# Optimization experiments

Hardware: AMD Instinct MI355X
Metric: run time of the kernel (lower is better)

## Reference

```python
import jax, jax.numpy as jnp
import numpy as np


def setup_inputs() -> dict:
    key = jax.random.key(0)
    k1, k2, k3 = jax.random.split(key, 3)
    b, n, d, f = 16, 2048, 256, 256
    features = jax.random.normal(k1, (b, n, d), dtype=jnp.float32)
    # dense adjacency; row-normalize like MeanAggregator's normalized A
    A = jax.random.uniform(k2, (b, n, n), dtype=jnp.float32)
    A = A / jnp.sum(A, axis=-1, keepdims=True)
    weight = jax.random.normal(k3, (2 * d, f), dtype=jnp.float32) * (1.0 / np.sqrt(2 * d))
    bias = jnp.zeros((f,), dtype=jnp.float32)
    return {"features": features, "A": A, "weight": weight, "bias": bias}


def reference(features, A, weight, bias):
    # agg = A @ features  (MeanAggregator: row-normalized adjacency)
    agg = jnp.einsum('bnm,bmd->bnd', A, features)  # [b,n,d]
    d = features.shape[-1]
    # split-weight GEMM instead of materializing concat:
    # [feat, agg] @ W == feat @ W[:d] + agg @ W[d:]
    out = (jnp.einsum('bnd,df->bnf', features, weight[:d])
           + jnp.einsum('bnd,df->bnf', agg, weight[d:])
           + bias)
    return jax.nn.relu(out)
```

## Files before the change

kernel.cpp:

```cpp
#include <hip/hip_runtime.h>

typedef __attribute__((ext_vector_type(8))) short bf16x8;
typedef __attribute__((ext_vector_type(4))) float f32x4;

__device__ __forceinline__ unsigned short f2bf(float f) {
    unsigned int u = __builtin_bit_cast(unsigned int, f);
    unsigned int r = (u + 0x7FFFu + ((u >> 16) & 1u)) >> 16;
    return (unsigned short)r;
}
__device__ __forceinline__ unsigned int pkbf(float lo, float hi) {
    unsigned int ul = __builtin_bit_cast(unsigned int, lo) + 0x8000u;
    unsigned int uh = __builtin_bit_cast(unsigned int, hi) + 0x8000u;
    return (uh & 0xFFFF0000u) | (ul >> 16);
}
__device__ __forceinline__ float bf2f(unsigned short u) {
    unsigned int x = ((unsigned int)u) << 16;
    return __builtin_bit_cast(float, x);
}

__device__ __forceinline__ void gll16(const void* g, void* l) {
    __builtin_amdgcn_global_load_lds(
        (const __attribute__((address_space(1))) void*)g,
        (__attribute__((address_space(3))) void*)l, 16, 0, 0);
}

__global__ __launch_bounds__(256) void transpose_cvt_kernel(
    const float* __restrict__ src, unsigned short* __restrict__ dstT,
    unsigned short* __restrict__ dstS, int R, int C)
{
    __shared__ float tile[64][65];
    const int b = blockIdx.z;
    const float* s = src + (size_t)b * R * C;
    const int r0 = blockIdx.x * 64, c0 = blockIdx.y * 64;
    const int t = threadIdx.x;
    const int r = t >> 2, cg = (t & 3) * 16;

    float v[16];
    const float4* p = reinterpret_cast<const float4*>(s + (size_t)(r0 + r) * C + c0 + cg);
#pragma unroll
    for (int i = 0; i < 4; ++i) {
        float4 q = p[i];
        v[4 * i + 0] = q.x; v[4 * i + 1] = q.y; v[4 * i + 2] = q.z; v[4 * i + 3] = q.w;
    }
#pragma unroll
    for (int i = 0; i < 16; ++i) tile[r][cg + i] = v[i];

    if (dstS) {
        unsigned int w[8];
#pragma unroll
        for (int i = 0; i < 8; ++i)
            w[i] = (unsigned)f2bf(v[2 * i]) | ((unsigned)f2bf(v[2 * i + 1]) << 16);
        unsigned int* d = reinterpret_cast<unsigned int*>(
            dstS + (size_t)b * R * C + (size_t)(r0 + r) * C + c0 + cg);
        *reinterpret_cast<uint4*>(d)     = make_uint4(w[0], w[1], w[2], w[3]);
        *reinterpret_cast<uint4*>(d + 4) = make_uint4(w[4], w[5], w[6], w[7]);
    }

    __syncthreads();

    const int cl = t >> 2, rg = (t & 3) * 16;
    unsigned int w[8];
#pragma unroll
    for (int i = 0; i < 8; ++i) {
        unsigned short lo = f2bf(tile[rg + 2 * i][cl]);
        unsigned short hi = f2bf(tile[rg + 2 * i + 1][cl]);
        w[i] = (unsigned)lo | ((unsigned)hi << 16);
    }
    unsigned int* d = reinterpret_cast<unsigned int*>(
        dstT + (size_t)b * R * C + (size_t)(c0 + cl) * R + r0 + rg);
    *reinterpret_cast<uint4*>(d)     = make_uint4(w[0], w[1], w[2], w[3]);
    *reinterpret_cast<uint4*>(d + 4) = make_uint4(w[4], w[5], w[6], w[7]);
}

__global__ __launch_bounds__(256, 2) void kpre_gemm(
    const float* __restrict__ F, const unsigned short* __restrict__ Wt,
    const float* __restrict__ bias, unsigned short* __restrict__ H,
    unsigned short* __restrict__ Gt)
{
    __shared__ __align__(16) short Fb[64 * 256];
    __shared__ __align__(16) short Wb[256 * 64];

    const int tid = threadIdx.x;
    const int lane = tid & 63, wid = tid >> 6;
    const int lo = lane & 15, hi = lane >> 4;
    const int rb = blockIdx.x;
    const int batch = rb >> 5;
    const int mb = (rb & 31) * 64;
    const size_t m0g = (size_t)rb * 64;

    {
        const int frow = tid >> 2, fq = tid & 3;
        const float* fp = F + (m0g + frow) * 256 + fq * 64;
#pragma unroll
        for (int g = 0; g < 2; ++g) {
            float4 q[8];
#pragma unroll
            for (int i = 0; i < 8; ++i)
                q[i] = reinterpret_cast<const float4*>(fp)[g * 8 + i];
#pragma unroll
            for (int j = 0; j < 4; ++j) {
                unsigned int w0 = pkbf(q[2*j].x,   q[2*j].y);
                unsigned int w1 = pkbf(q[2*j].z,   q[2*j].w);
                unsigned int w2 = pkbf(q[2*j+1].x, q[2*j+1].y);
                unsigned int w3 = pkbf(q[2*j+1].z, q[2*j+1].w);
                int slot = fq * 8 + g * 4 + j;
                int off = frow * 256 + ((slot ^ (frow & 7)) << 3);
                *reinterpret_cast<uint4*>(&Fb[off]) = make_uint4(w0, w1, w2, w3);
            }
        }
    }

    f32x4 acc[4][4];

#pragma unroll
    for (int pass = 0; pass < 2; ++pass) {
#pragma unroll
        for (int m = 0; m < 4; ++m)
#pragma unroll
            for (int n = 0; n < 4; ++n) acc[m][n] = (f32x4){0.f, 0.f, 0.f, 0.f};

        for (int kt = 0; kt < 4; ++kt) {
            const int kbase = pass * 256 + kt * 64;
#pragma unroll
            for (int it = 0; it < 8; ++it) {
                int si = it * 256 + tid;
                int row = si >> 3, slot = si & 7;
                const unsigned short* g = Wt + (size_t)row * 512 + kbase + ((slot ^ (row & 7)) << 3);
                gll16(g, Wb + (size_t)si * 8);
            }
            __syncthreads();

#pragma unroll
            for (int kk = 0; kk < 2; ++kk) {
                bf16x8 af[4], bw[4];
#pragma unroll
                for (int m = 0; m < 4; ++m) {
                    int row = m * 16 + lo;
                    int slot = kt * 8 + kk * 4 + hi;
                    af[m] = *reinterpret_cast<const bf16x8*>(&Fb[row * 256 + ((slot ^ (row & 7)) << 3)]);
                }
#pragma unroll
                for (int n = 0; n < 4; ++n) {
                    int row = wid * 64 + n * 16 + lo;
                    bw[n] = *reinterpret_cast<const bf16x8*>(&Wb[row * 64 + (((kk * 4 + hi) ^ (row & 7)) << 3)]);
                }
#pragma unroll
                for (int m = 0; m < 4; ++m)
#pragma unroll
                    for (int n = 0; n < 4; ++n)
                        acc[m][n] = __builtin_amdgcn_mfma_f32_16x16x32_bf16(af[m], bw[n], acc[m][n], 0, 0, 0);
            }
            __syncthreads();
        }

        if (pass == 0) {
            float bv[4];
#pragma unroll
            for (int n = 0; n < 4; ++n) bv[n] = bias[wid * 64 + n * 16 + lo];
            unsigned short* Hb = H + m0g * 256;
#pragma unroll
            for (int m = 0; m < 4; ++m)
#pragma unroll
                for (int n = 0; n < 4; ++n)
#pragma unroll
                    for (int j = 0; j < 4; ++j) {
                        int row = m * 16 + hi * 4 + j;
                        int col = wid * 64 + n * 16 + lo;
                        Hb[(size_t)row * 256 + col] = f2bf(acc[m][n][j] + bv[n]);
                    }
        } else {
            short* T = Wb + wid * 4096;
#pragma unroll
            for (int m = 0; m < 4; ++m)
#pragma unroll
                for (int n = 0; n < 4; ++n)
#pragma unroll
                    for (int j = 0; j < 4; ++j) {
                        int gr = m * 16 + hi * 4 + j;
                        int gc = n * 16 + lo;
                        int slot = gr >> 3, e = gr & 7;
                        T[gc * 64 + ((slot ^ (gc & 7)) << 3) + e] = f2bf(acc[m][n][j]);
                    }
            unsigned short* Gb = Gt + ((size_t)batch * 256 + wid * 64) * 2048 + mb;
#pragma unroll
            for (int i = 0; i < 8; ++i) {
                int f = i * 8 + (lane >> 3);
                int s = lane & 7;
                bf16x8 v = *reinterpret_cast<const bf16x8*>(&T[f * 64 + ((s ^ (f & 7)) << 3)]);
                *reinterpret_cast<bf16x8*>(Gb + (size_t)f * 2048 + s * 8) = v;
            }
        }
    }
}

__global__ __launch_bounds__(512, 2) void kmain_gemm(
    const float* __restrict__ A, const unsigned short* __restrict__ Gt,
    const unsigned short* __restrict__ H, float* __restrict__ out)
{
    __shared__ __align__(16) short Ab[2][128 * 64];
    __shared__ __align__(16) short Bb[2][256 * 64];

    const int tid = threadIdx.x;
    const int lane = tid & 63, wid = tid >> 6;
    const int wr = wid >> 2, wc = wid & 3;
    const int lo = lane & 15, hi = lane >> 4;

    const int bid = blockIdx.x;
    const int wg = ((bid & 7) << 5) | (bid >> 3);
    const int batch = wg >> 4;
    const int mt    = wg & 15;

    const float* Abase = A + ((size_t)batch * 2048 + (size_t)mt * 128) * 2048;
    const unsigned short* Gbase = Gt + (size_t)batch * 256 * 2048;

    const int arow = tid >> 2;
    const int acg  = tid & 3;

    f32x4 acc[4][4];
#pragma unroll
    for (int m = 0; m < 4; ++m)
#pragma unroll
        for (int n = 0; n < 4; ++n) acc[m][n] = (f32x4){0.f, 0.f, 0.f, 0.f};

    float4 qa0[4], qa1[4];

    auto loadA = [&](float4* q, int k0) {
        const float4* p4 = reinterpret_cast<const float4*>(
            Abase + (size_t)arow * 2048 + k0);
#pragma unroll
        for (int i = 0; i < 4; ++i) q[i] = p4[acg + 4 * i];
    };
    auto writeA = [&](int buf, const float4* q) {
#pragma unroll
        for (int i = 0; i < 4; ++i) {
            uint2 w;
            w.x = pkbf(q[i].x, q[i].y);
            w.y = pkbf(q[i].z, q[i].w);
            int s = 2 * i + (acg >> 1);
            int off = arow * 64 + ((s ^ (arow & 7)) << 3) + (acg & 1) * 4;
            *reinterpret_cast<uint2*>(&Ab[buf][off]) = w;
        }
    };
    auto stageB = [&](int buf, int k0) {
#pragma unroll
        for (int it = 0; it < 4; ++it) {
            int si = it * 512 + tid;
            int row = si >> 3, slot = si & 7;
            const unsigned short* g = Gbase + (size_t)row * 2048 + k0 + ((slot ^ (row & 7)) << 3);
            gll16(g, &Bb[buf][(size_t)si * 8]);
        }
    };
    auto compute = [&](int buf) {
#pragma unroll
        for (int kk = 0; kk < 2; ++kk) {
            bf16x8 af[4], bfv[4];
#pragma unroll
            for (int m = 0; m < 4; ++m) {
                int row = wr * 64 + m * 16 + lo;
                af[m] = *reinterpret_cast<const bf16x8*>(
                    &Ab[buf][row * 64 + (((kk * 4 + hi) ^ (row & 7)) << 3)]);
            }
#pragma unroll
            for (int n = 0; n < 4; ++n) {
                int row = wc * 64 + n * 16 + lo;
                bfv[n] = *reinterpret_cast<const bf16x8*>(
                    &Bb[buf][row * 64 + (((kk * 4 + hi) ^ (row & 7)) << 3)]);
            }
            __builtin_amdgcn_s_setprio(1);
#pragma unroll
            for (int m = 0; m < 4; ++m)
#pragma unroll
                for (int n = 0; n < 4; ++n)
                    acc[m][n] = __builtin_amdgcn_mfma_f32_16x16x32_bf16(af[m], bfv[n], acc[m][n], 0, 0, 0);
            __builtin_amdgcn_s_setprio(0);
        }
    };

    loadA(qa0, 0);
    stageB(0, 0);
    writeA(0, qa0);
    loadA(qa1, 64);
    asm volatile("s_waitcnt vmcnt(4) lgkmcnt(0)" ::: "memory");
    __builtin_amdgcn_s_barrier();
    asm volatile("" ::: "memory");
    stageB(1, 64);

    for (int tt = 0; tt < 15; ++tt) {
        const int t0 = tt * 2;
        writeA(1, qa1);
        loadA(qa0, (t0 + 2) * 64);
        compute(0);
        asm volatile("s_waitcnt vmcnt(4) lgkmcnt(0)" ::: "memory");
        __builtin_amdgcn_s_barrier();
        asm volatile("" ::: "memory");
        stageB(0, (t0 + 2) * 64);
        writeA(0, qa0);
        loadA(qa1, (t0 + 3) * 64);
        compute(1);
        asm volatile("s_waitcnt vmcnt(4) lgkmcnt(0)" ::: "memory");
        __builtin_amdgcn_s_barrier();
        asm volatile("" ::: "memory");
        stageB(1, (t0 + 3) * 64);
    }
    writeA(1, qa1);
    compute(0);
    asm volatile("s_waitcnt vmcnt(0) lgkmcnt(0)" ::: "memory");
    __builtin_amdgcn_s_barrier();
    asm volatile("" ::: "memory");
    compute(1);

    const size_t rowbase = (size_t)batch * 2048 + (size_t)mt * 128;
    const unsigned short* Hb = H + rowbase * 256;
    float* obase = out + rowbase * 256;
#pragma unroll
    for (int m = 0; m < 4; ++m) {
#pragma unroll
        for (int n = 0; n < 4; ++n) {
            int col = wc * 64 + n * 16 + lo;
#pragma unroll
            for (int j = 0; j < 4; ++j) {
                int row = wr * 64 + m * 16 + hi * 4 + j;
                float v = acc[m][n][j] + bf2f(Hb[(size_t)row * 256 + col]);
                obase[(size_t)row * 256 + col] = fmaxf(v, 0.f);
            }
        }
    }
}

extern "C" void kernel_launch(void* const* d_in, const int* in_sizes, int n_in,
                              void* d_out, int out_size, void* d_ws, size_t ws_size,
                              hipStream_t stream) {
    const float* features = (const float*)d_in[0];
    const float* A        = (const float*)d_in[1];
    const float* weight   = (const float*)d_in[2];
    const float* bias     = (const float*)d_in[3];
    float* out = (float*)d_out;

    const size_t WT_B = (size_t)256 * 512 * 2;
    const size_t H_B  = (size_t)32768 * 256 * 2;
    const size_t GT_B = (size_t)16 * 256 * 2048 * 2;
    if (ws_size < WT_B + H_B + GT_B) return;

    char* ws = (char*)d_ws;
    unsigned short* Wt = (unsigned short*)ws;
    unsigned short* H  = (unsigned short*)(ws + WT_B);
    unsigned short* Gt = (unsigned short*)(ws + WT_B + H_B);

    dim3 gW(512 / 64, 256 / 64, 1);
    transpose_cvt_kernel<<<gW, 256, 0, stream>>>(weight, Wt, nullptr, 512, 256);

    kpre_gemm<<<512, 256, 0, stream>>>(features, Wt, bias, H, Gt);

    kmain_gemm<<<256, 512, 0, stream>>>(A, Gt, H, out);
}
```

Before: 111.4 us.

## Split main GEMM output columns across two blocks with deeper K tiles

The main aggregation GEMM now tiles the output as 128x128 instead of 128x256, doubling the grid to 512 blocks, and raises the K step from 64 to 128 with a 16-slot XOR swizzle. The A-tile load is also reorganized so each wave reads whole rows with coalesced float4 accesses. The goal is more blocks in flight and fewer barriers per K. The cost is that each fp32 A row tile is now read and converted twice, once per column half, which doubles traffic on the largest input.

New measurement: 113.6 us. About the same (+2.0%).

```diff
diff --git a/kernel.cpp b/kernel.cpp
--- a/kernel.cpp
+++ b/kernel.cpp
@@ -197,8 +197,8 @@
     const float* __restrict__ A, const unsigned short* __restrict__ Gt,
     const unsigned short* __restrict__ H, float* __restrict__ out)
 {
-    __shared__ __align__(16) short Ab[2][128 * 64];
-    __shared__ __align__(16) short Bb[2][256 * 64];
+    __shared__ __align__(16) short Ab[2][128 * 128];
+    __shared__ __align__(16) short Bb[2][128 * 128];
 
     const int tid = threadIdx.x;
     const int lane = tid & 63, wid = tid >> 6;
@@ -206,38 +206,40 @@
     const int lo = lane & 15, hi = lane >> 4;
 
     const int bid = blockIdx.x;
-    const int wg = ((bid & 7) << 5) | (bid >> 3);
-    const int batch = wg >> 4;
-    const int mt    = wg & 15;
+    const int wg = ((bid & 7) << 6) | (bid >> 3);
+    const int batch = wg >> 5;
+    const int mt    = (wg >> 1) & 15;
+    const int nt    = wg & 1;
 
     const float* Abase = A + ((size_t)batch * 2048 + (size_t)mt * 128) * 2048;
-    const unsigned short* Gbase = Gt + (size_t)batch * 256 * 2048;
-
-    const int arow = tid >> 2;
-    const int acg  = tid & 3;
-
-    f32x4 acc[4][4];
+    const unsigned short* Gbase = Gt + ((size_t)batch * 256 + (size_t)nt * 128) * 2048;
+
+    f32x4 acc[4][2];
 #pragma unroll
     for (int m = 0; m < 4; ++m)
 #pragma unroll
-        for (int n = 0; n < 4; ++n) acc[m][n] = (f32x4){0.f, 0.f, 0.f, 0.f};
-
-    float4 qa0[4], qa1[4];
-
-    auto loadA = [&](float4* q, int k0) {
-        const float4* p4 = reinterpret_cast<const float4*>(
-            Abase + (size_t)arow * 2048 + k0);
-#pragma unroll
-        for (int i = 0; i < 4; ++i) q[i] = p4[acg + 4 * i];
+        for (int n = 0; n < 2; ++n) acc[m][n] = (f32x4){0.f, 0.f, 0.f, 0.f};
+
+    float4 qa[8];
+
+    auto loadA = [&](int k0) {
+        const float* base = Abase + k0;
+#pragma unroll
+        for (int i = 0; i < 8; ++i) {
+            int r = (wid << 4) + (i << 1) + (lane >> 5);
+            qa[i] = reinterpret_cast<const float4*>(base + (size_t)r * 2048)[lane & 31];
+        }
     };
-    auto writeA = [&](int buf, const float4* q) {
-#pragma unroll
-        for (int i = 0; i < 4; ++i) {
+    auto writeA = [&](int buf) {
+#pragma unroll
+        for (int i = 0; i < 8; ++i) {
+            int r = (wid << 4) + (i << 1) + (lane >> 5);
+            int c32 = lane & 31;
+            int slot = c32 >> 1, half = c32 & 1;
+            int off = r * 128 + (((slot ^ (r & 15)) << 3) + half * 4);
             uint2 w;
-            w.x = pkbf(q[i].x, q[i].y);
-            w.y = pkbf(q[i].z, q[i].w);
-            int s = 2 * i + (acg >> 1);
-            int off = arow * 64 + ((s ^ (arow & 7)) << 3) + (acg & 1) * 4;
+            w.x = pkbf(qa[i].x, qa[i].y);
+            w.y = pkbf(qa[i].z, qa[i].w);
             *reinterpret_cast<uint2*>(&Ab[buf][off]) = w;
         }
     };
@@ -245,64 +247,57 @@
 #pragma unroll
         for (int it = 0; it < 4; ++it) {
             int si = it * 512 + tid;
-            int row = si >> 3, slot = si & 7;
-            const unsigned short* g = Gbase + (size_t)row * 2048 + k0 + ((slot ^ (row & 7)) << 3);
+            int row = si >> 4, slot = si & 15;
+            const unsigned short* g = Gbase + (size_t)row * 2048 + k0 + ((slot ^ (row & 15)) << 3);
             gll16(g, &Bb[buf][(size_t)si * 8]);
         }
     };
     auto compute = [&](int buf) {
 #pragma unroll
-        for (int kk = 0; kk < 2; ++kk) {
-            bf16x8 af[4], bfv[4];
+        for (int kk = 0; kk < 4; ++kk) {
+            bf16x8 af[4], bfv[2];
 #pragma unroll
             for (int m = 0; m < 4; ++m) {
                 int row = wr * 64 + m * 16 + lo;
-                af[m] = *reinterpret_cast<const bf16x8*>(
-                    &Ab[buf][row * 64 + (((kk * 4 + hi) ^ (row & 7)) << 3)]);
-            }
-#pragma unroll
-            for (int n = 0; n < 4; ++n) {
-                int row = wc * 64 + n * 16 + lo;
-                bfv[n] = *reinterpret_cast<const bf16x8*>(
-                    &Bb[buf][row * 64 + (((kk * 4 + hi) ^ (row & 7)) << 3)]);
+                int s = (kk * 4 + hi) ^ (row & 15);
+                af[m] = *reinterpret_cast<const bf16x8*>(&Ab[buf][row * 128 + (s << 3)]);
+            }
+#pragma unroll
+            for (int n = 0; n < 2; ++n) {
+                int row = wc * 32 + n * 16 + lo;
+                int s = (kk * 4 + hi) ^ (row & 15);
+                bfv[n] = *reinterpret_cast<const bf16x8*>(&Bb[buf][row * 128 + (s << 3)]);
             }
             __builtin_amdgcn_s_setprio(1);
 #pragma unroll
             for (int m = 0; m < 4; ++m)
 #pragma unroll
-                for (int n = 0; n < 4; ++n)
+                for (int n = 0; n < 2; ++n)
                     acc[m][n] = __builtin_amdgcn_mfma_f32_16x16x32_bf16(af[m], bfv[n], acc[m][n], 0, 0, 0);
             __builtin_amdgcn_s_setprio(0);
         }
     };
 
-    loadA(qa0, 0);
+    loadA(0);
     stageB(0, 0);
-    writeA(0, qa0);
-    loadA(qa1, 64);
-    asm volatile("s_waitcnt vmcnt(4) lgkmcnt(0)" ::: "memory");
+    writeA(0);
+    loadA(128);
+    asm volatile("s_waitcnt vmcnt(8) lgkmcnt(0)" ::: "memory");
     __builtin_amdgcn_s_barrier();
     asm volatile("" ::: "memory");
-    stageB(1, 64);
-
-    for (int tt = 0; tt < 15; ++tt) {
-        const int t0 = tt * 2;
-        writeA(1, qa1);
-        loadA(qa0, (t0 + 2) * 64);
-        compute(0);
-        asm volatile("s_waitcnt vmcnt(4) lgkmcnt(0)" ::: "memory");
+    stageB(1, 128);
+
+    for (int t = 0; t < 14; ++t) {
+        const int cur = t & 1, nxt = cur ^ 1;
+        writeA(nxt);
+        loadA((t + 2) * 128);
+        compute(cur);
+        asm volatile("s_waitcnt vmcnt(8) lgkmcnt(0)" ::: "memory");
         __builtin_amdgcn_s_barrier();
         asm volatile("" ::: "memory");
-        stageB(0, (t0 + 2) * 64);
-        writeA(0, qa0);
-        loadA(qa1, (t0 + 3) * 64);
-        compute(1);
-        asm volatile("s_waitcnt vmcnt(4) lgkmcnt(0)" ::: "memory");
-        __builtin_amdgcn_s_barrier();
-        asm volatile("" ::: "memory");
-        stageB(1, (t0 + 3) * 64);
-    }
-    writeA(1, qa1);
+        stageB(cur, (t + 2) * 128);
+    }
+    writeA(1);
     compute(0);
     asm volatile("s_waitcnt vmcnt(0) lgkmcnt(0)" ::: "memory");
     __builtin_amdgcn_s_barrier();
@@ -315,8 +310,8 @@
 #pragma unroll
     for (int m = 0; m < 4; ++m) {
 #pragma unroll
-        for (int n = 0; n < 4; ++n) {
-            int col = wc * 64 + n * 16 + lo;
+        for (int n = 0; n < 2; ++n) {
+            int col = nt * 128 + wc * 32 + n * 16 + lo;
 #pragma unroll
             for (int j = 0; j < 4; ++j) {
                 int row = wr * 64 + m * 16 + hi * 4 + j;
@@ -351,5 +346,5 @@
 
     kpre_gemm<<<512, 256, 0, stream>>>(features, Wt, bias, H, Gt);
 
-    kmain_gemm<<<256, 512, 0, stream>>>(A, Gt, H, out);
-}
+    kmain_gemm<<<512, 512, 0, stream>>>(A, Gt, H, out);
+}
```
